# Kernel tuning notes

Hardware: AMD Instinct MI355X
Metric: run time of the kernel (lower is better)

Reference implementation:

```python
import jax, jax.numpy as jnp
import numpy as np

B, C, H, W = 8, 256, 64, 64
N = 3  # num_param
EPS = 1e-5


def conv2d(x, w, b=None, stride=(1, 1), padding=((0, 0), (0, 0)), dilation=(1, 1), groups=1):
    out = jax.lax.conv_general_dilated(
        x, w, window_strides=stride, padding=padding, rhs_dilation=dilation,
        dimension_numbers=('NCHW', 'OIHW', 'NCHW'), feature_group_count=groups)
    if b is not None:
        out = out + b[None, :, None, None]
    return out


def akconv(x, p_w, p_b, ak_w, ak_gamma, ak_beta):
    b, c, h, w = x.shape
    offset = conv2d(x, p_w, p_b, padding=((1, 1), (1, 1)))  # (b, 2N, h, w)
    # initial kernel offsets p_n for num_param=3: rows [0,0,1], cols [0,1,0]
    p_n = jnp.concatenate([jnp.array([0., 0., 1.]), jnp.array([0., 1., 0.])]).reshape(1, 2 * N, 1, 1)
    gx = jnp.broadcast_to(jnp.arange(h, dtype=x.dtype)[:, None], (h, w))
    gy = jnp.broadcast_to(jnp.arange(w, dtype=x.dtype)[None, :], (h, w))
    p_0 = jnp.concatenate([jnp.tile(gx[None, None], (1, N, 1, 1)),
                           jnp.tile(gy[None, None], (1, N, 1, 1))], axis=1)  # (1, 2N, h, w)
    p = p_0 + p_n + offset                      # (b, 2N, h, w)
    p = jnp.transpose(p, (0, 2, 3, 1))          # (b, h, w, 2N)
    q = jnp.floor(jax.lax.stop_gradient(p))
    q_lt_x = jnp.clip(q[..., :N], 0, h - 1)
    q_lt_y = jnp.clip(q[..., N:], 0, w - 1)
    q_rb_x = jnp.clip(q[..., :N] + 1, 0, h - 1)
    q_rb_y = jnp.clip(q[..., N:] + 1, 0, w - 1)
    px = jnp.clip(p[..., :N], 0, h - 1)
    py = jnp.clip(p[..., N:], 0, w - 1)
    # bilinear weights (b, h, w, N)
    g_lt = (1 + (q_lt_x - px)) * (1 + (q_lt_y - py))
    g_rb = (1 - (q_rb_x - px)) * (1 - (q_rb_y - py))
    g_lb = (1 + (q_lt_x - px)) * (1 - (q_rb_y - py))
    g_rt = (1 - (q_rb_x - px)) * (1 + (q_lt_y - py))

    x_flat = x.reshape(b, c, h * w)

    def gather(qx, qy):
        idx = (qx * w + qy).astype(jnp.int32).reshape(b, -1)  # (b, h*w*N)
        out = jnp.take_along_axis(x_flat, idx[:, None, :], axis=2)
        return out.reshape(b, c, h, w, N)

    x_off = (g_lt[:, None] * gather(q_lt_x, q_lt_y)
             + g_rb[:, None] * gather(q_rb_x, q_rb_y)
             + g_lb[:, None] * gather(q_lt_x, q_rb_y)
             + g_rt[:, None] * gather(q_rb_x, q_lt_y))   # (b, c, h, w, N)
    # rearrange 'b c h w n -> b c (h n) w'
    x_off = jnp.transpose(x_off, (0, 1, 2, 4, 3)).reshape(b, c, h * N, w)
    out = conv2d(x_off, ak_w, None, stride=(N, 1))        # (b, c, h, w)
    # BatchNorm2d in training mode (batch statistics) + SiLU
    mean = out.mean(axis=(0, 2, 3), keepdims=True)
    var = ((out - mean) ** 2).mean(axis=(0, 2, 3), keepdims=True)
    out = (out - mean) / jnp.sqrt(var + EPS) * ak_gamma[None, :, None, None] + ak_beta[None, :, None, None]
    return jax.nn.silu(out)


def lka(x, w0, b0, ws, bs, w1, b1):
    u = x
    attn = conv2d(x, w0, b0, padding=((2, 2), (2, 2)), groups=C)                       # 5x5 depthwise
    attn = conv2d(attn, ws, bs, padding=((9, 9), (9, 9)), dilation=(3, 3), groups=C)   # 7x7 dw, dil 3
    attn = conv2d(attn, w1, b1)                                                        # 1x1
    return u * attn


def setup_inputs() -> dict:
    key = jax.random.key(0)
    ks = jax.random.split(key, 8)
    return {
        'x': jax.random.normal(ks[0], (B, C, H, W), jnp.float32),
        'p_w': jax.random.normal(ks[1], (2 * N, C, 3, 3), jnp.float32) * 0.01,
        'p_b': jnp.zeros((2 * N,), jnp.float32),
        'ak_w': jax.random.normal(ks[2], (C, C, 3, 1), jnp.float32) * 0.05,
        'ak_gamma': jnp.ones((C,), jnp.float32),
        'ak_beta': jnp.zeros((C,), jnp.float32),
        'lka0_w': jax.random.normal(ks[3], (C, 1, 5, 5), jnp.float32) * 0.05,
        'lka0_b': jnp.zeros((C,), jnp.float32),
        'lkas_w': jax.random.normal(ks[4], (C, 1, 7, 7), jnp.float32) * 0.05,
        'lkas_b': jnp.zeros((C,), jnp.float32),
        'lka1_w': jax.random.normal(ks[5], (C, C, 1, 1), jnp.float32) * 0.05,
        'lka1_b': jnp.zeros((C,), jnp.float32),
        'conv_w': jax.random.normal(ks[6], (C, C, 1, 1), jnp.float32) * 0.05,
        'conv_b': jnp.zeros((C,), jnp.float32),
    }


def reference(x, p_w, p_b, ak_w, ak_gamma, ak_beta, lka0_w, lka0_b, lkas_w, lkas_b, lka1_w, lka1_b, conv_w, conv_b):
    res = x
    y = akconv(x, p_w, p_b, ak_w, ak_gamma, ak_beta)
    y = lka(y, lka0_w, lka0_b, lkas_w, lkas_b, lka1_w, lka1_b)
    y = conv2d(y, conv_w, conv_b)
    return y + res
```

## Files before the change

kernel.cpp:

```cpp
#include <hip/hip_runtime.h>
#include <math.h>
#include <stdint.h>

#define B_ 8
#define C_ 256
#define HW_ 4096
#define NPIX 32768
#define NELEM (B_*C_*HW_)

typedef __attribute__((ext_vector_type(8))) short short8;
typedef __attribute__((ext_vector_type(4))) float f32x4;

__device__ __forceinline__ unsigned short f2bf(float f) {
    union { float f; uint32_t u; } v; v.f = f;
    uint32_t r = v.u + 0x7FFFu + ((v.u >> 16) & 1u);
    return (unsigned short)(r >> 16);
}
__device__ __forceinline__ float b2f(unsigned short h) {
    union { uint32_t u; float f; } v; v.u = ((uint32_t)h) << 16; return v.f;
}
__device__ __forceinline__ float silu_f(float v) { return v / (1.f + __expf(-v)); }

__device__ __forceinline__ float4 up4(uint2 v) {
    float4 r;
    r.x = b2f((unsigned short)(v.x & 0xffffu));
    r.y = b2f((unsigned short)(v.x >> 16));
    r.z = b2f((unsigned short)(v.y & 0xffffu));
    r.w = b2f((unsigned short)(v.y >> 16));
    return r;
}

__device__ __forceinline__ void gl2lds16(const void* g, void* l) {
    __builtin_amdgcn_global_load_lds(
        (const __attribute__((address_space(1))) void*)g,
        (__attribute__((address_space(3))) void*)l,
        16, 0, 0);
}

__global__ __launch_bounds__(256) void prep_kernel(
    const float* __restrict__ akw, const float* __restrict__ l1w,
    const float* __restrict__ cvw, const float* __restrict__ pw,
    unsigned short* __restrict__ wak, unsigned short* __restrict__ wl1,
    unsigned short* __restrict__ wcv, float* __restrict__ pwt)
{
    int gid = blockIdx.x * 256 + threadIdx.x;
    if (gid < 196608) {
        int e = gid & 7;
        int co = (gid >> 3) & 255;
        int q = gid >> 11;
        int kpp = q * 8 + e;
        int n = kpp >> 8, ci = kpp & 255;
        wak[gid] = f2bf(akw[co * 768 + ci * 3 + n]);
    }
    else if (gid < 262144) {
        int g = gid - 196608;
        int e = g & 7, co = (g >> 3) & 255, q = g >> 11;
        wl1[g] = f2bf(l1w[co * 256 + q * 8 + e]);
    }
    else if (gid < 327680) {
        int g = gid - 262144;
        int e = g & 7, co = (g >> 3) & 255, q = g >> 11;
        wcv[g] = f2bf(cvw[co * 256 + q * 8 + e]);
    }
    else if (gid < 346112) {
        int idx = gid - 327680;
        int ci = idx / 72, r = idx - ci * 72;
        int tt = r / 12, t9 = r - tt * 12;
        pwt[idx] = (t9 < 9) ? pw[tt * 2304 + ci * 9 + t9] : 0.f;
    }
}

__global__ __launch_bounds__(256) void transpose_kernel(
    const float* __restrict__ x, unsigned short* __restrict__ xt)
{
    int blk = blockIdx.x;
    int b = blk & 7;
    int rest = blk >> 3;
    int half = rest & 1, i = rest >> 1;
    int bi = b * 64 + i;
    int tid = threadIdx.x;
    __shared__ float tile[64 * 132];

    {
        int ci_l = tid >> 6, jj = tid & 63;
        const float* ip = x + ((size_t)b * C_ + half * 128 + ci_l) * HW_ + i * 64 + jj;
        #pragma unroll 4
        for (int it = 0; it < 32; ++it)
            tile[jj * 132 + ci_l + it * 4] = ip[(size_t)it * 4 * HW_];
    }
    __syncthreads();
    {
        int j = tid >> 2, q = tid & 3;
        unsigned short* op = xt + ((size_t)(bi * 64 + j)) * 256 + half * 128 + q * 32;
        const float* tp = &tile[j * 132 + q * 32];
        #pragma unroll
        for (int f = 0; f < 4; ++f) {
            union { unsigned short h[8]; uint4 u; } pk;
            #pragma unroll
            for (int e = 0; e < 8; ++e) pk.h[e] = f2bf(tp[f * 8 + e]);
            *(uint4*)(op + f * 8) = pk.u;
        }
    }
}

__global__ __launch_bounds__(256) void offset_s1_kernel(
    const float* __restrict__ x, const float* __restrict__ pwt,
    float* __restrict__ part)
{
    int blk = blockIdx.x;
    int b = blk & 7;
    int rest = blk >> 3;
    int g = rest & 7, i = rest >> 3;
    int bi = b * 64 + i;
    int tid = threadIdx.x;

    __shared__ float tile[6600];

    {
        int cs = tid >> 3, r8 = tid & 7;
        const float* xp = x + ((size_t)b * C_ + g * 32 + cs) * HW_;
        #pragma unroll
        for (int t = 0; t < 6; ++t) {
            int idx = r8 * 6 + t;
            int r = idx >> 4, v4 = idx & 15;
            int ii = i + r - 1;
            float4 val = make_float4(0.f, 0.f, 0.f, 0.f);
            if (ii >= 0 && ii < 64)
                val = *(const float4*)(xp + ii * 64 + v4 * 4);
            int base = (r * 66 + 1 + v4 * 4) * 33 + cs;
            tile[base]      = val.x;  tile[base + 33]  = val.y;
            tile[base + 66] = val.z;  tile[base + 99]  = val.w;
        }
        if (tid < 192) {
            int ci = tid / 6, rem = tid - ci * 6;
            int ki = rem >> 1, side = rem & 1;
            tile[(ki * 66 + side * 65) * 33 + ci] = 0.f;
        }
    }
    __syncthreads();

    int sub = tid >> 4;
    int jq  = tid & 15;

    float acc[6][4];
    #pragma unroll
    for (int tt = 0; tt < 6; ++tt)
        #pragma unroll
        for (int p = 0; p < 4; ++p) acc[tt][p] = 0.f;

    #pragma unroll
    for (int t = 0; t < 2; ++t) {
        int ci = sub + 16 * t;
        float xv[3][6];
        #pragma unroll
        for (int ki = 0; ki < 3; ++ki)
            #pragma unroll
            for (int cc = 0; cc < 6; ++cc)
                xv[ki][cc] = tile[(ki * 66 + jq * 4 + cc) * 33 + ci];
        const float* wp = pwt + (g * 32 + ci) * 72;
        #pragma unroll
        for (int tt = 0; tt < 6; ++tt) {
            float w[9];
            *(float4*)&w[0] = *(const float4*)(wp + tt * 12);
            *(float4*)&w[4] = *(const float4*)(wp + tt * 12 + 4);
            w[8] = wp[tt * 12 + 8];
            #pragma unroll
            for (int ki = 0; ki < 3; ++ki)
                #pragma unroll
                for (int kj = 0; kj < 3; ++kj) {
                    float wgt = w[ki * 3 + kj];
                    #pragma unroll
                    for (int p = 0; p < 4; ++p)
                        acc[tt][p] += wgt * xv[ki][kj + p];
                }
        }
    }

    __syncthreads();
    {
        float* s2 = tile + sub * 387;
        #pragma unroll
        for (int tt = 0; tt < 6; ++tt)
            #pragma unroll
            for (int p = 0; p < 4; ++p)
                s2[tt * 64 + jq * 4 + p] = acc[tt][p];
    }
    __syncthreads();
    size_t pslot = (size_t)bi * 8 + g;
    for (int idx = tid; idx < 384; idx += 256) {
        float s = 0.f;
        #pragma unroll
        for (int sb = 0; sb < 16; ++sb)
            s += tile[sb * 387 + idx];
        part[pslot * 384 + idx] = s;
    }
}

__global__ __launch_bounds__(256) void offset_s2_kernel(
    const float* __restrict__ part, const float* __restrict__ pb,
    int2* __restrict__ tbl_off, float4* __restrict__ tbl_w)
{
    int pix = blockIdx.x * 256 + threadIdx.x;
    int b = pix >> 12, rem = pix & 4095, i = rem >> 6, j = rem & 63;
    int bi = b * 64 + i;
    float v[6];
    #pragma unroll
    for (int tt = 0; tt < 6; ++tt) v[tt] = pb[tt];
    for (int g = 0; g < 8; ++g) {
        const float* pp = part + ((size_t)bi * 8 + g) * 384;
        #pragma unroll
        for (int tt = 0; tt < 6; ++tt) v[tt] += pp[tt * 64 + j];
    }
    const float pnx[3] = {0.f, 0.f, 1.f};
    const float pny[3] = {0.f, 1.f, 0.f};
    #pragma unroll
    for (int n = 0; n < 3; ++n) {
        float px_ = (float)i + pnx[n] + v[n];
        float py_ = (float)j + pny[n] + v[n + 3];
        float qx = floorf(px_), qy = floorf(py_);
        float qlx = fminf(fmaxf(qx,       0.f), 63.f);
        float qly = fminf(fmaxf(qy,       0.f), 63.f);
        float qrx = fminf(fmaxf(qx + 1.f, 0.f), 63.f);
        float qry = fminf(fmaxf(qy + 1.f, 0.f), 63.f);
        float pxc = fminf(fmaxf(px_,      0.f), 63.f);
        float pyc = fminf(fmaxf(py_,      0.f), 63.f);
        float glt = (1.f + (qlx - pxc)) * (1.f + (qly - pyc));
        float grb = (1.f - (qrx - pxc)) * (1.f - (qry - pyc));
        float glb = (1.f + (qlx - pxc)) * (1.f - (qry - pyc));
        float grt = (1.f - (qrx - pxc)) * (1.f + (qly - pyc));
        int ilx = (int)qlx, irx = (int)qrx;
        int ily = (int)qly, iry = (int)qry;
        int c0; float a0, a1, b0, b1;
        if (ily == iry) {
            if (ily == 0) { c0 = 0;  a0 = glt + glb; a1 = 0.f; b0 = grt + grb; b1 = 0.f; }
            else          { c0 = 62; a0 = 0.f; a1 = glt + glb; b0 = 0.f; b1 = grt + grb; }
        } else { c0 = ily; a0 = glt; a1 = glb; b0 = grt; b1 = grb; }
        int oi = (b * 3 + n) * HW_ + i * 64 + j;
        tbl_off[oi] = make_int2(ilx * 64 + c0, irx * 64 + c0);
        tbl_w[oi]   = make_float4(a0, a1, b0, b1);
    }
}

__global__ __launch_bounds__(256) void gather_kernel(
    const unsigned short* __restrict__ xt, const int2* __restrict__ tbl_off,
    const float4* __restrict__ tbl_w, unsigned short* __restrict__ v)
{
    int blk = blockIdx.x;
    int b = blk & 7;
    int rest = blk >> 3;
    int n = rest >> 6, i = rest & 63;
    int bi = b * 64 + i;
    int tid = threadIdx.x;
    int lane = tid & 63, wv = tid >> 6;
    int ci4 = lane * 4;
    const unsigned short* xb = xt + (size_t)b * 1048576;

    __shared__ unsigned short stile[16640];
    int tCloc = ci4 >> 5;
    int kq = (ci4 >> 3) & 3;
    int e  = ci4 & 7;
    unsigned short* sl = &stile[tCloc * 2080 + kq * 520 + e];

    for (int it0 = 0; it0 < 16; it0 += 4) {
        uint2 A8[4], B8[4], C8[4], D8[4];
        float4 w4[4];
        #pragma unroll
        for (int u = 0; u < 4; ++u) {
            int j = wv * 16 + it0 + u;
            int oi = (b * 3 + n) * HW_ + i * 64 + j;
            int2 off = tbl_off[oi];
            w4[u] = tbl_w[oi];
            const unsigned short* p0 = xb + (size_t)off.x * 256 + ci4;
            const unsigned short* p1 = xb + (size_t)off.y * 256 + ci4;
            A8[u] = *(const uint2*)p0;
            B8[u] = *(const uint2*)(p0 + 256);
            C8[u] = *(const uint2*)p1;
            D8[u] = *(const uint2*)(p1 + 256);
        }
        #pragma unroll
        for (int u = 0; u < 4; ++u) {
            int j = wv * 16 + it0 + u;
            float4 A = up4(A8[u]), Bv = up4(B8[u]), Cv = up4(C8[u]), Dv = up4(D8[u]);
            union { unsigned short h[4]; uint2 q; } pk;
            pk.h[0] = f2bf(w4[u].x*A.x + w4[u].y*Bv.x + w4[u].z*Cv.x + w4[u].w*Dv.x);
            pk.h[1] = f2bf(w4[u].x*A.y + w4[u].y*Bv.y + w4[u].z*Cv.y + w4[u].w*Dv.y);
            pk.h[2] = f2bf(w4[u].x*A.z + w4[u].y*Bv.z + w4[u].z*Cv.z + w4[u].w*Dv.z);
            pk.h[3] = f2bf(w4[u].x*A.w + w4[u].y*Bv.w + w4[u].z*Cv.w + w4[u].w*Dv.w);
            *(uint2*)&sl[j * 8] = pk.q;
        }
    }
    __syncthreads();
    unsigned short* vb = v + ((size_t)bi * 24 + n * 8) * 2048;
    int kqW = tid >> 6, jW = tid & 63;
    #pragma unroll
    for (int tc = 0; tc < 8; ++tc) {
        *(uint4*)&vb[tc * 2048 + kqW * 512 + jW * 8] =
            *(const uint4*)&stile[tc * 2080 + kqW * 520 + jW * 8];
    }
}

__global__ __launch_bounds__(256) void ak_mfma_kernel(
    const unsigned short* __restrict__ v, const unsigned short* __restrict__ W,
    unsigned short* __restrict__ yh, float* __restrict__ p1, float* __restrict__ p2)
{
    int blk = blockIdx.x;
    int b = blk & 7, i = blk >> 3;
    int P = b * 64 + i;
    int tid = threadIdx.x;
    int wv = tid >> 6, lane = tid & 63;
    int quad = lane >> 4, l15 = lane & 15;
    __shared__ __align__(16) unsigned short sA[8192];
    __shared__ __align__(16) unsigned short sB[2048];

    const unsigned short* vP = v + (size_t)P * 24 * 2048;

    f32x4 acc[4][4];
    #pragma unroll
    for (int mt = 0; mt < 4; ++mt)
        #pragma unroll
        for (int nt = 0; nt < 4; ++nt) acc[mt][nt] = (f32x4){0.f, 0.f, 0.f, 0.f};

    for (int t = 0; t < 24; ++t) {
        #pragma unroll
        for (int s = 0; s < 4; ++s)
            gl2lds16(W + ((size_t)(t * 4 + s) * 256 + tid) * 8, &sA[(s * 256 + tid) * 8]);
        gl2lds16(vP + (size_t)t * 2048 + tid * 8, &sB[tid * 8]);
        __syncthreads();
        short8 af[4], bf[4];
        #pragma unroll
        for (int mt = 0; mt < 4; ++mt)
            af[mt] = *(const short8*)&sA[(quad * 256 + wv * 64 + mt * 16 + l15) * 8];
        #pragma unroll
        for (int nt = 0; nt < 4; ++nt)
            bf[nt] = *(const short8*)&sB[(quad * 64 + nt * 16 + l15) * 8];
        #pragma unroll
        for (int mt = 0; mt < 4; ++mt)
            #pragma unroll
            for (int nt = 0; nt < 4; ++nt)
                acc[mt][nt] = __builtin_amdgcn_mfma_f32_16x16x32_bf16(
                    af[mt], bf[nt], acc[mt][nt], 0, 0, 0);
        __syncthreads();
    }
    #pragma unroll
    for (int mt = 0; mt < 4; ++mt) {
        #pragma unroll
        for (int r = 0; r < 4; ++r) {
            int co = wv * 64 + mt * 16 + quad * 4 + r;
            size_t base = ((size_t)b * C_ + co) * HW_ + i * 64;
            float s1 = 0.f, s2 = 0.f;
            #pragma unroll
            for (int nt = 0; nt < 4; ++nt) {
                float val = acc[mt][nt][r];
                s1 += val; s2 += val * val;
                yh[base + nt * 16 + l15] = f2bf(val);
            }
            #pragma unroll
            for (int m = 1; m < 16; m <<= 1) {
                s1 += __shfl_xor(s1, m); s2 += __shfl_xor(s2, m);
            }
            if (l15 == 0) { p1[co * 512 + blk] = s1; p2[co * 512 + blk] = s2; }
        }
    }
}

__global__ __launch_bounds__(256) void bn_stats_kernel(
    const float* __restrict__ p1, const float* __restrict__ p2,
    const float* __restrict__ gamma, const float* __restrict__ beta,
    float* __restrict__ ss)
{
    int co = blockIdx.x, tid = threadIdx.x;
    float a = p1[co * 512 + tid] + p1[co * 512 + 256 + tid];
    float q = p2[co * 512 + tid] + p2[co * 512 + 256 + tid];
    __shared__ float r1[256], r2[256];
    r1[tid] = a; r2[tid] = q; __syncthreads();
    for (int st = 128; st > 0; st >>= 1) {
        if (tid < st) { r1[tid] += r1[tid + st]; r2[tid] += r2[tid + st]; }
        __syncthreads();
    }
    if (tid == 0) {
        const float inv_n = 1.f / (float)NPIX;
        float m = r1[0] * inv_n;
        float var = r2[0] * inv_n - m * m;
        float sc = gamma[co] * rsqrtf(var + 1e-5f);
        ss[co] = sc; ss[256 + co] = beta[co] - m * sc;
    }
}

__global__ __launch_bounds__(256) void dw5_fused_kernel(
    const unsigned short* __restrict__ in, const float* __restrict__ ss,
    const float* __restrict__ w, const float* __restrict__ bias,
    unsigned short* __restrict__ out)
{
    int blkI = blockIdx.x;
    int b = blkI & 7, c = blkI >> 3;
    int bc = b * 256 + c;
    int tid = threadIdx.x;
    __shared__ float tile[68 * 68];
    float sc = ss[c], sh = ss[256 + c];
    const unsigned short* ip = in + (size_t)bc * HW_;
    for (int s = tid; s < 68 * 68; s += 256) {
        int r = s / 68, cc = s - r * 68;
        int ii = r - 2, jj = cc - 2;
        float vv = 0.f;
        if (ii >= 0 && ii < 64 && jj >= 0 && jj < 64) {
            float t = b2f(ip[ii * 64 + jj]) * sc + sh;
            vv = silu_f(t);
        }
        tile[s] = vv;
    }
    float wr[25];
    #pragma unroll
    for (int t = 0; t < 25; ++t) wr[t] = w[c * 25 + t];
    float bv = bias[c];
    __syncthreads();

    int jb = tid & 3, row = tid >> 2;
    int j0 = jb * 16;
    float acc[16];
    #pragma unroll
    for (int j = 0; j < 16; ++j) acc[j] = bv;
    #pragma unroll
    for (int di = 0; di < 5; ++di) {
        const float* tp = &tile[(row + di) * 68 + j0];
        float vv[20];
        #pragma unroll
        for (int q = 0; q < 5; ++q)
            *(float4*)&vv[q * 4] = *(const float4*)(tp + q * 4);
        #pragma unroll
        for (int dj = 0; dj < 5; ++dj) {
            float wv = wr[di * 5 + dj];
            #pragma unroll
            for (int j = 0; j < 16; ++j)
                acc[j] += wv * vv[dj + j];
        }
    }
    unsigned short* op = out + (size_t)bc * HW_ + row * 64 + j0;
    union { unsigned short h[8]; uint4 u; } pk;
    #pragma unroll
    for (int half = 0; half < 2; ++half) {
        #pragma unroll
        for (int j = 0; j < 8; ++j) pk.h[j] = f2bf(acc[half * 8 + j]);
        *(uint4*)&op[half * 8] = pk.u;
    }
}

__global__ __launch_bounds__(256) void dw7d3_kernel(
    const unsigned short* __restrict__ in, const float* __restrict__ w,
    const float* __restrict__ bias, unsigned short* __restrict__ out)
{
    int blkI = blockIdx.x;
    int b = blkI & 7, c = blkI >> 3;
    int bc = b * 256 + c;
    int tid = threadIdx.x;
    __shared__ float tile[82 * 84];
    const unsigned short* ip = in + (size_t)bc * HW_;
    for (int s = tid; s < 82 * 84; s += 256) {
        int r = s / 84, cc = s - r * 84;
        int ii = r - 9, jj = cc - 9;
        float vv = 0.f;
        if (ii >= 0 && ii < 64 && jj >= 0 && jj < 64) vv = b2f(ip[ii * 64 + jj]);
        tile[s] = vv;
    }
    float wr[49];
    #pragma unroll
    for (int t = 0; t < 49; ++t) wr[t] = w[c * 49 + t];
    float bv = bias[c];
    __syncthreads();

    int jb = tid & 3, row = tid >> 2;
    int j0 = jb * 16;
    float acc[16];
    #pragma unroll
    for (int j = 0; j < 16; ++j) acc[j] = bv;
    #pragma unroll
    for (int di = 0; di < 7; ++di) {
        const float* tp = &tile[(row + 3 * di) * 84 + j0];
        float vv[36];
        #pragma unroll
        for (int q = 0; q < 9; ++q)
            *(float4*)&vv[q * 4] = *(const float4*)(tp + q * 4);
        #pragma unroll
        for (int dj = 0; dj < 7; ++dj) {
            float wv = wr[di * 7 + dj];
            #pragma unroll
            for (int j = 0; j < 16; ++j)
                acc[j] += wv * vv[3 * dj + j];
        }
    }
    unsigned short* op = out + (size_t)bc * HW_ + row * 64 + j0;
    union { unsigned short h[8]; uint4 u; } pk;
    #pragma unroll
    for (int half = 0; half < 2; ++half) {
        #pragma unroll
        for (int j = 0; j < 8; ++j) pk.h[j] = f2bf(acc[half * 8 + j]);
        *(uint4*)&op[half * 8] = pk.u;
    }
}

__global__ __launch_bounds__(256) void gemm_fused_kernel(
    const unsigned short* __restrict__ in,
    const unsigned short* __restrict__ W0, const float* __restrict__ bias0,
    const unsigned short* __restrict__ W1, const float* __restrict__ bias1,
    const unsigned short* __restrict__ auxh, const float* __restrict__ ss,
    const float* __restrict__ auxf, float* __restrict__ out_f)
{
    int blk = blockIdx.x;
    int b = blk & 7, i = blk >> 3;
    int tid = threadIdx.x;
    int wv = tid >> 6, lane = tid & 63;
    int quad = lane >> 4, l15 = lane & 15;
    __shared__ __align__(16) unsigned short sA[8192];
    __shared__ __align__(16) unsigned short sB[2048];
    __shared__ __align__(16) unsigned short mid[16384];
    int pixS = tid & 63, kqS = tid >> 6;

    const unsigned short* bp = in + ((size_t)b * C_) * HW_ + i * 64 + pixS;

    f32x4 acc[4][4];
    #pragma unroll
    for (int mt = 0; mt < 4; ++mt)
        #pragma unroll
        for (int nt = 0; nt < 4; ++nt) acc[mt][nt] = (f32x4){0.f, 0.f, 0.f, 0.f};

    for (int t = 0; t < 8; ++t) {
        #pragma unroll
        for (int s = 0; s < 4; ++s)
            gl2lds16(W0 + ((size_t)(t * 4 + s) * 256 + tid) * 8, &sA[(s * 256 + tid) * 8]);
        {
            const unsigned short* p = bp + (size_t)(t * 32 + kqS * 8) * HW_;
            union { unsigned short h[8]; uint4 u; } hb;
            #pragma unroll
            for (int jj = 0; jj < 8; ++jj) hb.h[jj] = p[(size_t)jj * HW_];
            *(uint4*)&sB[(kqS * 64 + pixS) * 8] = hb.u;
        }
        __syncthreads();
        short8 af[4], bf[4];
        #pragma unroll
        for (int mt = 0; mt < 4; ++mt)
            af[mt] = *(const short8*)&sA[(quad * 256 + wv * 64 + mt * 16 + l15) * 8];
        #pragma unroll
        for (int nt = 0; nt < 4; ++nt)
            bf[nt] = *(const short8*)&sB[(quad * 64 + nt * 16 + l15) * 8];
        #pragma unroll
        for (int mt = 0; mt < 4; ++mt)
            #pragma unroll
            for (int nt = 0; nt < 4; ++nt)
                acc[mt][nt] = __builtin_amdgcn_mfma_f32_16x16x32_bf16(
                    af[mt], bf[nt], acc[mt][nt], 0, 0, 0);
        __syncthreads();
    }
    #pragma unroll
    for (int mt = 0; mt < 4; ++mt) {
        #pragma unroll
        for (int r = 0; r < 4; ++r) {
            int co = wv * 64 + mt * 16 + quad * 4 + r;
            float bco = bias0[co];
            size_t base = ((size_t)b * C_ + co) * HW_ + i * 64;
            float sc = ss[co], sh = ss[256 + co];
            #pragma unroll
            for (int nt = 0; nt < 4; ++nt) {
                int col = nt * 16 + l15;
                float o = acc[mt][nt][r] + bco;
                float u = silu_f(b2f(auxh[base + col]) * sc + sh);
                mid[((co >> 3) * 64 + col) * 8 + (co & 7)] = f2bf(o * u);
            }
        }
    }
    #pragma unroll
    for (int mt = 0; mt < 4; ++mt)
        #pragma unroll
        for (int nt = 0; nt < 4; ++nt) acc[mt][nt] = (f32x4){0.f, 0.f, 0.f, 0.f};
    for (int t = 0; t < 8; ++t) {
        #pragma unroll
        for (int s = 0; s < 4; ++s)
            gl2lds16(W1 + ((size_t)(t * 4 + s) * 256 + tid) * 8, &sA[(s * 256 + tid) * 8]);
        __syncthreads();
        short8 af[4], bf[4];
        #pragma unroll
        for (int mt = 0; mt < 4; ++mt)
            af[mt] = *(const short8*)&sA[(quad * 256 + wv * 64 + mt * 16 + l15) * 8];
        #pragma unroll
        for (int nt = 0; nt < 4; ++nt)
            bf[nt] = *(const short8*)&mid[((t * 4 + quad) * 64 + nt * 16 + l15) * 8];
        #pragma unroll
        for (int mt = 0; mt < 4; ++mt)
            #pragma unroll
            for (int nt = 0; nt < 4; ++nt)
                acc[mt][nt] = __builtin_amdgcn_mfma_f32_16x16x32_bf16(
                    af[mt], bf[nt], acc[mt][nt], 0, 0, 0);
        __syncthreads();
    }
    #pragma unroll
    for (int mt = 0; mt < 4; ++mt) {
        #pragma unroll
        for (int r = 0; r < 4; ++r) {
            int co = wv * 64 + mt * 16 + quad * 4 + r;
            float bco = bias1[co];
            size_t base = ((size_t)b * C_ + co) * HW_ + i * 64;
            #pragma unroll
            for (int nt = 0; nt < 4; ++nt) {
                int col = nt * 16 + l15;
                out_f[base + col] = acc[mt][nt][r] + bco + auxf[base + col];
            }
        }
    }
}

extern "C" void kernel_launch(void* const* d_in, const int* in_sizes, int n_in,
                              void* d_out, int out_size, void* d_ws, size_t ws_size,
                              hipStream_t stream) {
    const float* x     = (const float*)d_in[0];
    const float* p_w   = (const float*)d_in[1];
    const float* p_b   = (const float*)d_in[2];
    const float* ak_w  = (const float*)d_in[3];
    const float* ak_g  = (const float*)d_in[4];
    const float* ak_b  = (const float*)d_in[5];
    const float* l0_w  = (const float*)d_in[6];
    const float* l0_b  = (const float*)d_in[7];
    const float* ls_w  = (const float*)d_in[8];
    const float* ls_b  = (const float*)d_in[9];
    const float* l1_w  = (const float*)d_in[10];
    const float* l1_b  = (const float*)d_in[11];
    const float* cv_w  = (const float*)d_in[12];
    const float* cv_b  = (const float*)d_in[13];
    float* out = (float*)d_out;

    char* w = (char*)d_ws;
    int2*   tbl_off = (int2*)w;
    float4* tbl_w   = (float4*)(w + 786432);
    unsigned short* wak = (unsigned short*)(w + 2359296);
    unsigned short* wl1 = (unsigned short*)(w + 2752512);
    unsigned short* wcv = (unsigned short*)(w + 2883584);
    float* p1 = (float*)(w + 3014656);
    float* p2 = (float*)(w + 3538944);
    float* ss = (float*)(w + 4063232);
    float* pwt = (float*)(w + 4065280);
    unsigned short* xt = (unsigned short*)(w + 4194304);
    unsigned short* ybh    = (unsigned short*)(w + 4194304);
    unsigned short* dw5out = (unsigned short*)(w + 20971520);
    float* part = (float*)(w + 37748736);
    unsigned short* attn   = (unsigned short*)(w + 37748736);
    unsigned short* v      = (unsigned short*)(w + 44040192);

    prep_kernel<<<1352, 256, 0, stream>>>(ak_w, l1_w, cv_w, p_w, wak, wl1, wcv, pwt);
    offset_s1_kernel<<<4096, 256, 0, stream>>>(x, pwt, part);
    offset_s2_kernel<<<128, 256, 0, stream>>>(part, p_b, tbl_off, tbl_w);
    transpose_kernel<<<1024, 256, 0, stream>>>(x, xt);
    gather_kernel<<<1536, 256, 0, stream>>>(xt, tbl_off, tbl_w, v);
    ak_mfma_kernel<<<512, 256, 0, stream>>>(v, wak, ybh, p1, p2);
    bn_stats_kernel<<<256, 256, 0, stream>>>(p1, p2, ak_g, ak_b, ss);
    dw5_fused_kernel<<<2048, 256, 0, stream>>>(ybh, ss, l0_w, l0_b, dw5out);
    dw7d3_kernel<<<2048, 256, 0, stream>>>(dw5out, ls_w, ls_b, attn);
    gemm_fused_kernel<<<512, 256, 0, stream>>>(attn, wl1, l1_b, wcv, cv_b, ybh, ss, x, out);
}
```

Before: 272.9 us.

## Merge transpose into prep kernel, split AK GEMM over output channels, deepen gather unroll

The separate transpose kernel is folded into the weight prep kernel as extra blocks, which removes one launch. The gather loop now issues 8 pixels of loads per batch instead of 4, raising memory-level parallelism at the cost of more registers. The AK MFMA kernel splits the 256 output channels across two blocks, doubling the grid to 1024 for better occupancy. In exchange, the v tile is loaded twice and per-block MFMA reuse drops.

```diff
diff --git a/kernel.cpp b/kernel.cpp
--- a/kernel.cpp
+++ b/kernel.cpp
@@ -37,13 +37,44 @@
         16, 0, 0);
 }
 
-__global__ __launch_bounds__(256) void prep_kernel(
+__global__ __launch_bounds__(256) void prep_transpose_kernel(
     const float* __restrict__ akw, const float* __restrict__ l1w,
     const float* __restrict__ cvw, const float* __restrict__ pw,
     unsigned short* __restrict__ wak, unsigned short* __restrict__ wl1,
-    unsigned short* __restrict__ wcv, float* __restrict__ pwt)
-{
-    int gid = blockIdx.x * 256 + threadIdx.x;
+    unsigned short* __restrict__ wcv, float* __restrict__ pwt,
+    const float* __restrict__ x, unsigned short* __restrict__ xt)
+{
+    __shared__ float tile[64 * 132];
+    int blk = blockIdx.x;
+    int tid = threadIdx.x;
+    if (blk < 1024) {
+        int b = blk & 7;
+        int rest = blk >> 3;
+        int half = rest & 1, i = rest >> 1;
+        int bi = b * 64 + i;
+        {
+            int ci_l = tid >> 6, jj = tid & 63;
+            const float* ip = x + ((size_t)b * C_ + half * 128 + ci_l) * HW_ + i * 64 + jj;
+            #pragma unroll 4
+            for (int it = 0; it < 32; ++it)
+                tile[jj * 132 + ci_l + it * 4] = ip[(size_t)it * 4 * HW_];
+        }
+        __syncthreads();
+        {
+            int j = tid >> 2, q = tid & 3;
+            unsigned short* op = xt + ((size_t)(bi * 64 + j)) * 256 + half * 128 + q * 32;
+            const float* tp = &tile[j * 132 + q * 32];
+            #pragma unroll
+            for (int f = 0; f < 4; ++f) {
+                union { unsigned short h[8]; uint4 u; } pk;
+                #pragma unroll
+                for (int e = 0; e < 8; ++e) pk.h[e] = f2bf(tp[f * 8 + e]);
+                *(uint4*)(op + f * 8) = pk.u;
+            }
+        }
+        return;
+    }
+    int gid = (blk - 1024) * 256 + tid;
     if (gid < 196608) {
         int e = gid & 7;
         int co = (gid >> 3) & 255;
@@ -67,39 +98,6 @@
         int ci = idx / 72, r = idx - ci * 72;
         int tt = r / 12, t9 = r - tt * 12;
         pwt[idx] = (t9 < 9) ? pw[tt * 2304 + ci * 9 + t9] : 0.f;
-    }
-}
-
-__global__ __launch_bounds__(256) void transpose_kernel(
-    const float* __restrict__ x, unsigned short* __restrict__ xt)
-{
-    int blk = blockIdx.x;
-    int b = blk & 7;
-    int rest = blk >> 3;
-    int half = rest & 1, i = rest >> 1;
-    int bi = b * 64 + i;
-    int tid = threadIdx.x;
-    __shared__ float tile[64 * 132];
-
-    {
-        int ci_l = tid >> 6, jj = tid & 63;
-        const float* ip = x + ((size_t)b * C_ + half * 128 + ci_l) * HW_ + i * 64 + jj;
-        #pragma unroll 4
-        for (int it = 0; it < 32; ++it)
-            tile[jj * 132 + ci_l + it * 4] = ip[(size_t)it * 4 * HW_];
-    }
-    __syncthreads();
-    {
-        int j = tid >> 2, q = tid & 3;
-        unsigned short* op = xt + ((size_t)(bi * 64 + j)) * 256 + half * 128 + q * 32;
-        const float* tp = &tile[j * 132 + q * 32];
-        #pragma unroll
-        for (int f = 0; f < 4; ++f) {
-            union { unsigned short h[8]; uint4 u; } pk;
-            #pragma unroll
-            for (int e = 0; e < 8; ++e) pk.h[e] = f2bf(tp[f * 8 + e]);
-            *(uint4*)(op + f * 8) = pk.u;
-        }
     }
 }
 
@@ -261,11 +259,11 @@
     int e  = ci4 & 7;
     unsigned short* sl = &stile[tCloc * 2080 + kq * 520 + e];
 
-    for (int it0 = 0; it0 < 16; it0 += 4) {
-        uint2 A8[4], B8[4], C8[4], D8[4];
-        float4 w4[4];
-        #pragma unroll
-        for (int u = 0; u < 4; ++u) {
+    for (int it0 = 0; it0 < 16; it0 += 8) {
+        uint2 A8[8], B8[8], C8[8], D8[8];
+        float4 w4[8];
+        #pragma unroll
+        for (int u = 0; u < 8; ++u) {
             int j = wv * 16 + it0 + u;
             int oi = (b * 3 + n) * HW_ + i * 64 + j;
             int2 off = tbl_off[oi];
@@ -278,7 +276,7 @@
             D8[u] = *(const uint2*)(p1 + 256);
         }
         #pragma unroll
-        for (int u = 0; u < 4; ++u) {
+        for (int u = 0; u < 8; ++u) {
             int j = wv * 16 + it0 + u;
             float4 A = up4(A8[u]), Bv = up4(B8[u]), Cv = up4(C8[u]), Dv = up4(D8[u]);
             union { unsigned short h[4]; uint2 q; } pk;
@@ -303,38 +301,44 @@
     const unsigned short* __restrict__ v, const unsigned short* __restrict__ W,
     unsigned short* __restrict__ yh, float* __restrict__ p1, float* __restrict__ p2)
 {
-    int blk = blockIdx.x;
-    int b = blk & 7, i = blk >> 3;
-    int P = b * 64 + i;
+    int pid = blockIdx.x;
+    int mt2 = (pid >> 3) & 1;
+    int rest = (pid & 7) | ((pid >> 4) << 3);
+    int b = rest & 7, i = rest >> 3;
+    int co0 = mt2 * 128;
     int tid = threadIdx.x;
     int wv = tid >> 6, lane = tid & 63;
     int quad = lane >> 4, l15 = lane & 15;
-    __shared__ __align__(16) unsigned short sA[8192];
+    __shared__ __align__(16) unsigned short sA[4096];
     __shared__ __align__(16) unsigned short sB[2048];
 
-    const unsigned short* vP = v + (size_t)P * 24 * 2048;
-
-    f32x4 acc[4][4];
-    #pragma unroll
-    for (int mt = 0; mt < 4; ++mt)
+    const unsigned short* vP = v + (size_t)(b * 64 + i) * 24 * 2048;
+    int cS = tid & 127, hS = tid >> 7;
+
+    f32x4 acc[2][4];
+    #pragma unroll
+    for (int mt = 0; mt < 2; ++mt)
         #pragma unroll
         for (int nt = 0; nt < 4; ++nt) acc[mt][nt] = (f32x4){0.f, 0.f, 0.f, 0.f};
 
     for (int t = 0; t < 24; ++t) {
         #pragma unroll
-        for (int s = 0; s < 4; ++s)
-            gl2lds16(W + ((size_t)(t * 4 + s) * 256 + tid) * 8, &sA[(s * 256 + tid) * 8]);
+        for (int s = 0; s < 2; ++s) {
+            int chunk = hS * 2 + s;
+            gl2lds16(W + ((size_t)(t * 4 + chunk) * 256 + co0 + cS) * 8,
+                     &sA[(chunk * 128 + cS) * 8]);
+        }
         gl2lds16(vP + (size_t)t * 2048 + tid * 8, &sB[tid * 8]);
         __syncthreads();
-        short8 af[4], bf[4];
-        #pragma unroll
-        for (int mt = 0; mt < 4; ++mt)
-            af[mt] = *(const short8*)&sA[(quad * 256 + wv * 64 + mt * 16 + l15) * 8];
+        short8 af[2], bf[4];
+        #pragma unroll
+        for (int mt = 0; mt < 2; ++mt)
+            af[mt] = *(const short8*)&sA[(quad * 128 + wv * 32 + mt * 16 + l15) * 8];
         #pragma unroll
         for (int nt = 0; nt < 4; ++nt)
             bf[nt] = *(const short8*)&sB[(quad * 64 + nt * 16 + l15) * 8];
         #pragma unroll
-        for (int mt = 0; mt < 4; ++mt)
+        for (int mt = 0; mt < 2; ++mt)
             #pragma unroll
             for (int nt = 0; nt < 4; ++nt)
                 acc[mt][nt] = __builtin_amdgcn_mfma_f32_16x16x32_bf16(
@@ -342,10 +346,10 @@
         __syncthreads();
     }
     #pragma unroll
-    for (int mt = 0; mt < 4; ++mt) {
+    for (int mt = 0; mt < 2; ++mt) {
         #pragma unroll
         for (int r = 0; r < 4; ++r) {
-            int co = wv * 64 + mt * 16 + quad * 4 + r;
+            int co = co0 + wv * 32 + mt * 16 + quad * 4 + r;
             size_t base = ((size_t)b * C_ + co) * HW_ + i * 64;
             float s1 = 0.f, s2 = 0.f;
             #pragma unroll
@@ -358,7 +362,7 @@
             for (int m = 1; m < 16; m <<= 1) {
                 s1 += __shfl_xor(s1, m); s2 += __shfl_xor(s2, m);
             }
-            if (l15 == 0) { p1[co * 512 + blk] = s1; p2[co * 512 + blk] = s2; }
+            if (l15 == 0) { p1[co * 512 + rest] = s1; p2[co * 512 + rest] = s2; }
         }
     }
 }
@@ -642,12 +646,12 @@
     unsigned short* attn   = (unsigned short*)(w + 37748736);
     unsigned short* v      = (unsigned short*)(w + 44040192);
 
-    prep_kernel<<<1352, 256, 0, stream>>>(ak_w, l1_w, cv_w, p_w, wak, wl1, wcv, pwt);
+    prep_transpose_kernel<<<2376, 256, 0, stream>>>(ak_w, l1_w, cv_w, p_w,
+                                                    wak, wl1, wcv, pwt, x, xt);
     offset_s1_kernel<<<4096, 256, 0, stream>>>(x, pwt, part);
     offset_s2_kernel<<<128, 256, 0, stream>>>(part, p_b, tbl_off, tbl_w);
-    transpose_kernel<<<1024, 256, 0, stream>>>(x, xt);
     gather_kernel<<<1536, 256, 0, stream>>>(xt, tbl_off, tbl_w, v);
-    ak_mfma_kernel<<<512, 256, 0, stream>>>(v, wak, ybh, p1, p2);
+    ak_mfma_kernel<<<1024, 256, 0, stream>>>(v, wak, ybh, p1, p2);
     bn_stats_kernel<<<256, 256, 0, stream>>>(p1, p2, ak_g, ak_b, ss);
     dw5_fused_kernel<<<2048, 256, 0, stream>>>(ybh, ss, l0_w, l0_b, dw5out);
     dw7d3_kernel<<<2048, 256, 0, stream>>>(dw5out, ls_w, ls_b, attn);
```

New measurement: 266.8 us. -2.2%, faster.
